# Kernel tuning notes

Hardware: AMD Instinct MI355X
Metric: run time of the kernel (lower is better)

Reference implementation:

```python
import jax, jax.numpy as jnp
import numpy as np

N = 50000      # nodes
E = 640000     # edges
D = 128        # input_dim
H = 128        # hidden_channels
L = 2          # n_layers
NG = 512       # number of graphs
NC = 1         # n_classes
BN_EPS = 1e-5


def _bn(x, gamma, beta):
    # BatchNorm1d over node dim, batch statistics (biased var), eps=1e-5
    mu = jnp.mean(x, axis=0)
    var = jnp.mean((x - mu) ** 2, axis=0)
    return (x - mu) * jax.lax.rsqrt(var + BN_EPS) * gamma + beta


def setup_inputs() -> dict:
    key = jax.random.key(0)
    ks = jax.random.split(key, 16)
    s = 0.05
    x = jax.random.normal(ks[0], (N, D), dtype=jnp.float32)
    edge_index = jax.random.randint(ks[1], (2, E), 0, N, dtype=jnp.int64)
    batch = jnp.sort(jax.random.randint(ks[2], (N,), 0, NG, dtype=jnp.int64))
    return {
        "x": x,
        "edge_index": edge_index,
        "batch": batch,
        "lin_in_w": jax.random.normal(ks[3], (D, H), dtype=jnp.float32) * s,
        "lin_in_b": jnp.zeros((H,), dtype=jnp.float32),
        "mlp_w1": jax.random.normal(ks[4], (L, H, H), dtype=jnp.float32) * s,
        "mlp_b1": jnp.zeros((L, H), dtype=jnp.float32),
        "bn1_g": jnp.ones((L, H), dtype=jnp.float32),
        "bn1_b": jnp.zeros((L, H), dtype=jnp.float32),
        "mlp_w2": jax.random.normal(ks[5], (L, H, H), dtype=jnp.float32) * s,
        "mlp_b2": jnp.zeros((L, H), dtype=jnp.float32),
        "bn_g": jnp.ones((L, H), dtype=jnp.float32),
        "bn_b": jnp.zeros((L, H), dtype=jnp.float32),
        "jk_w": jax.random.normal(ks[6], (L * H, NC), dtype=jnp.float32) * s,
        "jk_b": jnp.zeros((NC,), dtype=jnp.float32),
    }


def reference(x, edge_index, batch, lin_in_w, lin_in_b, mlp_w1, mlp_b1,
              bn1_g, bn1_b, mlp_w2, mlp_b2, bn_g, bn_b, jk_w, jk_b):
    src, dst = edge_index[0], edge_index[1]
    n = x.shape[0]
    h = x @ lin_in_w + lin_in_b  # [N, H]
    outs = []
    for l in range(mlp_w1.shape[0]):
        # GINConv (eps=0): mlp(x + sum_{j in N(i)} x_j)
        agg = jax.ops.segment_sum(h[src], dst, num_segments=n)
        z = h + agg
        z = z @ mlp_w1[l] + mlp_b1[l]
        z = jax.nn.relu(_bn(z, bn1_g[l], bn1_b[l]))
        z = z @ mlp_w2[l] + mlp_b2[l]
        # outer BatchNorm + ReLU; dropout is identity in eval
        h = jax.nn.relu(_bn(z, bn_g[l], bn_b[l]))
        outs.append(h)
    hcat = jnp.concatenate(outs, axis=-1)  # [N, L*H]
    # global mean pool per graph
    counts = jax.ops.segment_sum(jnp.ones((n,), dtype=hcat.dtype), batch, num_segments=NG)
    pooled = jax.ops.segment_sum(hcat, batch, num_segments=NG)
    pooled = pooled / jnp.maximum(counts, 1.0)[:, None]
    return pooled @ jk_w + jk_b  # [NG, n_classes]
```

## Files before the change

### kernel.cpp

```cpp
#include <hip/hip_runtime.h>
#include <cstddef>

#define NN 50000
#define NE 640000
#define NG 512
#define NL 2
#define NSLOT 16
constexpr float BN_EPS = 1e-5f;

typedef __attribute__((ext_vector_type(8))) short bf16x8;
typedef __attribute__((ext_vector_type(16))) float f32x16;

__device__ inline float b2f_lo(unsigned int u) {
  union { unsigned int i; float f; } v; v.i = u << 16; return v.f;
}
__device__ inline float b2f_hi(unsigned int u) {
  union { unsigned int i; float f; } v; v.i = u & 0xffff0000u; return v.f;
}
__device__ inline unsigned short f2b(float f) {
  union { float f; unsigned int i; } v; v.f = f;
  return (unsigned short)((v.i + 0x7fffu + ((v.i >> 16) & 1u)) >> 16);
}
__device__ inline unsigned int pack2(float lo, float hi) {
  return (unsigned int)f2b(lo) | ((unsigned int)f2b(hi) << 16);
}
__device__ inline int swz(int row, int b) { return row * 256 + (b ^ ((row & 15) << 4)); }

__device__ inline void unpack_add(const uint4 v, float* a) {
  a[0] += b2f_lo(v.x); a[1] += b2f_hi(v.x); a[2] += b2f_lo(v.y); a[3] += b2f_hi(v.y);
  a[4] += b2f_lo(v.z); a[5] += b2f_hi(v.z); a[6] += b2f_lo(v.w); a[7] += b2f_hi(v.w);
}

template <int MODE, bool STATS>
__global__ __launch_bounds__(256) void gemm_fused(
    const void* __restrict__ Ain, const float* __restrict__ scale,
    const float* __restrict__ shift, const int* __restrict__ rowptr,
    const int* __restrict__ srcs, const unsigned short* __restrict__ Wt,
    const float* __restrict__ bias, unsigned short* __restrict__ C,
    float* __restrict__ psum, float* __restrict__ psq, int n) {
  __shared__ char Al[16384];
  __shared__ float colsum[128];
  __shared__ float colsq[128];
  const int t = threadIdx.x;
  const int row0 = blockIdx.x * 64;

  if (STATS && t < 128) { colsum[t] = 0.f; colsq[t] = 0.f; }

  if (MODE == 1) {
    const uint4* h4 = (const uint4*)Ain;
    const int ln = t >> 2;
    const int tq = t & 3;
    const int gr = row0 + ln;
    float a[4][8];
    #pragma unroll
    for (int i = 0; i < 4; ++i)
      #pragma unroll
      for (int p = 0; p < 8; ++p) a[i][p] = 0.f;
    if (gr < n) {
      {
        const uint4* p = &h4[(size_t)gr * 16 + tq * 4];
        #pragma unroll
        for (int i = 0; i < 4; ++i) unpack_add(p[i], a[i]);
      }
      const int beg = rowptr[gr], end = rowptr[gr + 1];
      int j = beg;
      for (; j + 1 < end; j += 2) {
        const uint4* p0 = &h4[(size_t)srcs[j] * 16 + tq * 4];
        const uint4* p1 = &h4[(size_t)srcs[j + 1] * 16 + tq * 4];
        const uint4 v00 = p0[0], v01 = p0[1], v02 = p0[2], v03 = p0[3];
        const uint4 v10 = p1[0], v11 = p1[1], v12 = p1[2], v13 = p1[3];
        unpack_add(v00, a[0]); unpack_add(v01, a[1]);
        unpack_add(v02, a[2]); unpack_add(v03, a[3]);
        unpack_add(v10, a[0]); unpack_add(v11, a[1]);
        unpack_add(v12, a[2]); unpack_add(v13, a[3]);
      }
      if (j < end) {
        const uint4* p0 = &h4[(size_t)srcs[j] * 16 + tq * 4];
        #pragma unroll
        for (int i = 0; i < 4; ++i) unpack_add(p0[i], a[i]);
      }
    }
    #pragma unroll
    for (int i = 0; i < 4; ++i) {
      uint4 o;
      o.x = pack2(a[i][0], a[i][1]); o.y = pack2(a[i][2], a[i][3]);
      o.z = pack2(a[i][4], a[i][5]); o.w = pack2(a[i][6], a[i][7]);
      *(uint4*)(Al + swz(ln, (tq * 4 + i) * 16)) = o;
    }
  } else {
    #pragma unroll
    for (int ii = 0; ii < 4; ++ii) {
      const int i = t + ii * 256;
      const int r = i >> 4;
      const int u = (i & 15) << 4;
      const int gr = row0 + r;
      uint4 v = make_uint4(0u, 0u, 0u, 0u);
      if (gr < n) {
        if (MODE == 3) {
          const float* Af = (const float*)Ain;
          const float4 f0 = *(const float4*)(Af + (size_t)gr * 128 + (u >> 1));
          const float4 f1 = *(const float4*)(Af + (size_t)gr * 128 + (u >> 1) + 4);
          v.x = pack2(f0.x, f0.y); v.y = pack2(f0.z, f0.w);
          v.z = pack2(f1.x, f1.y); v.w = pack2(f1.z, f1.w);
        } else {
          v = *(const uint4*)((const char*)Ain + (size_t)gr * 256 + u);
          if (MODE == 2) {
            const int c0 = u >> 1;
            unsigned int pw[4] = {v.x, v.y, v.z, v.w};
            #pragma unroll
            for (int p = 0; p < 4; ++p) {
              float lo = b2f_lo(pw[p]);
              float hi = b2f_hi(pw[p]);
              lo = fmaxf(fmaf(lo, scale[c0 + 2 * p], shift[c0 + 2 * p]), 0.f);
              hi = fmaxf(fmaf(hi, scale[c0 + 2 * p + 1], shift[c0 + 2 * p + 1]), 0.f);
              pw[p] = pack2(lo, hi);
            }
            v = make_uint4(pw[0], pw[1], pw[2], pw[3]);
          }
        }
      }
      *(uint4*)(Al + swz(r, u)) = v;
    }
  }
  __syncthreads();

  const int w = t >> 6;
  const int l = t & 63;
  const int lane31 = l & 31;
  const int khalf = l >> 5;
  const int mrow = (w & 1) * 32;
  const int c0 = (w >> 1) * 64;

  f32x16 acc0, acc1;
  #pragma unroll
  for (int i = 0; i < 16; ++i) { acc0[i] = 0.f; acc1[i] = 0.f; }

  const unsigned short* Bp0 = Wt + (size_t)(c0 + lane31) * 128 + 8 * khalf;
  const unsigned short* Bp1 = Wt + (size_t)(c0 + 32 + lane31) * 128 + 8 * khalf;

  #pragma unroll
  for (int k0 = 0; k0 < 128; k0 += 16) {
    const int kb = (k0 + 8 * khalf) * 2;
    const bf16x8 a  = *(const bf16x8*)(Al + swz(mrow + lane31, kb));
    const bf16x8 b0 = *(const bf16x8*)(Bp0 + k0);
    const bf16x8 b1 = *(const bf16x8*)(Bp1 + k0);
    acc0 = __builtin_amdgcn_mfma_f32_32x32x16_bf16(a, b0, acc0, 0, 0, 0);
    acc1 = __builtin_amdgcn_mfma_f32_32x32x16_bf16(a, b1, acc1, 0, 0, 0);
  }

  const float bias0 = bias[c0 + lane31];
  const float bias1 = bias[c0 + 32 + lane31];
  float s0 = 0.f, q0 = 0.f, s1 = 0.f, q1 = 0.f;
  #pragma unroll
  for (int r = 0; r < 16; ++r) {
    const int row = mrow + (r & 3) + 8 * (r >> 2) + 4 * khalf;
    const int grow = row0 + row;
    if (grow < n) {
      const float v0 = acc0[r] + bias0;
      const float v1 = acc1[r] + bias1;
      C[(size_t)grow * 128 + c0 + lane31] = f2b(v0);
      C[(size_t)grow * 128 + c0 + 32 + lane31] = f2b(v1);
      if (STATS) {
        s0 += v0; q0 = fmaf(v0, v0, q0);
        s1 += v1; q1 = fmaf(v1, v1, q1);
      }
    }
  }
  if (STATS) {
    atomicAdd(&colsum[c0 + lane31], s0);
    atomicAdd(&colsq[c0 + lane31], q0);
    atomicAdd(&colsum[c0 + 32 + lane31], s1);
    atomicAdd(&colsq[c0 + 32 + lane31], q1);
    __syncthreads();
    if (t < 128) {
      const int slot = blockIdx.x & (NSLOT - 1);
      atomicAdd(&psum[slot * 128 + t], colsum[t]);
      atomicAdd(&psq[slot * 128 + t], colsq[t]);
    }
  }
}

__global__ __launch_bounds__(256) void conv_w_k(
    const float* __restrict__ lw, const float* __restrict__ w1,
    const float* __restrict__ w2, unsigned short* __restrict__ Wt) {
  const int i = blockIdx.x * 256 + threadIdx.x;
  if (i >= 5 * 16384) return;
  const int m = i >> 14, r = i & 16383;
  const int ncol = r >> 7, k = r & 127;
  const float* src = (m == 0) ? lw : (m <= 2) ? (w1 + (m - 1) * 16384)
                                              : (w2 + (m - 3) * 16384);
  Wt[i] = f2b(src[k * 128 + ncol]);
}

#define SCAN_B 196
__global__ __launch_bounds__(256) void edge_hist(const int* __restrict__ ei,
                                                 int* __restrict__ cnt) {
  const int e = blockIdx.x * 256 + threadIdx.x;
  if (e >= NE) return;
  atomicAdd(&cnt[ei[NE + e]], 1);
}

__global__ __launch_bounds__(256) void scan1(const int* __restrict__ cnt,
                                             int* __restrict__ rowptr,
                                             int* __restrict__ bsum) {
  __shared__ int s[256];
  const int b = blockIdx.x, t = threadIdx.x;
  const int i = b * 256 + t;
  const int v = (i < NN) ? cnt[i] : 0;
  s[t] = v;
  __syncthreads();
  for (int off = 1; off < 256; off <<= 1) {
    const int x = (t >= off) ? s[t - off] : 0;
    __syncthreads();
    s[t] += x;
    __syncthreads();
  }
  if (i < NN) rowptr[i] = s[t] - v;
  if (t == 255) bsum[b] = s[255];
}

__global__ __launch_bounds__(256) void scan2(const int* __restrict__ bsum,
                                             int* __restrict__ boff,
                                             int* __restrict__ rowptrN) {
  __shared__ int s[256];
  const int t = threadIdx.x;
  const int v = (t < SCAN_B) ? bsum[t] : 0;
  s[t] = v;
  __syncthreads();
  for (int off = 1; off < 256; off <<= 1) {
    const int x = (t >= off) ? s[t - off] : 0;
    __syncthreads();
    s[t] += x;
    __syncthreads();
  }
  if (t < SCAN_B) boff[t] = s[t] - v;
  if (t == 255) *rowptrN = s[255];
}

__global__ __launch_bounds__(256) void scan3(int* __restrict__ rowptr,
                                             const int* __restrict__ boff,
                                             int* __restrict__ cursor) {
  const int i = blockIdx.x * 256 + threadIdx.x;
  if (i < NN) {
    const int v = rowptr[i] + boff[blockIdx.x];
    rowptr[i] = v;
    cursor[i] = v;
  }
}

__global__ __launch_bounds__(256) void build_csr(const int* __restrict__ ei,
                                                 int* __restrict__ cursor,
                                                 int* __restrict__ srcs) {
  const int e = blockIdx.x * 256 + threadIdx.x;
  if (e >= NE) return;
  const int src = ei[e];
  const int dst = ei[NE + e];
  const int pos = atomicAdd(&cursor[dst], 1);
  srcs[pos] = src;
}

__global__ void bn_stats_final(const float* __restrict__ psum,
                               const float* __restrict__ psq,
                               const float* __restrict__ gamma,
                               const float* __restrict__ beta,
                               float* __restrict__ scale,
                               float* __restrict__ shift, int n) {
  const int c = threadIdx.x;
  float s = 0.f, s2 = 0.f;
  #pragma unroll
  for (int b = 0; b < NSLOT; ++b) {
    s += psum[b * 128 + c];
    s2 += psq[b * 128 + c];
  }
  const float inv_n = 1.f / (float)n;
  const float mu = s * inv_n;
  float var = s2 * inv_n - mu * mu;
  var = fmaxf(var, 0.f);
  const float sc = rsqrtf(var + BN_EPS) * gamma[c];
  scale[c] = sc;
  shift[c] = beta[c] - mu * sc;
}

template <bool WRITE_H>
__global__ __launch_bounds__(256) void bn_relu_pool_seg_b(
    const unsigned short* __restrict__ Z, const float* __restrict__ scale,
    const float* __restrict__ shift, const int* __restrict__ gstart,
    unsigned short* __restrict__ h, float* __restrict__ pooled, int layerOff) {
  const int g = blockIdx.x;
  const int r0 = gstart[g], r1 = gstart[g + 1];
  const int t = threadIdx.x;
  const int q = t & 15;
  const int rr = t >> 4;
  const int c0 = q * 8;
  float sc[8], sh[8], acc[8];
  #pragma unroll
  for (int i = 0; i < 8; ++i) { sc[i] = scale[c0 + i]; sh[i] = shift[c0 + i]; acc[i] = 0.f; }
  for (int r = r0 + rr; r < r1; r += 16) {
    const uint4 v = ((const uint4*)Z)[(size_t)r * 16 + q];
    float o[8];
    o[0] = b2f_lo(v.x); o[1] = b2f_hi(v.x); o[2] = b2f_lo(v.y); o[3] = b2f_hi(v.y);
    o[4] = b2f_lo(v.z); o[5] = b2f_hi(v.z); o[6] = b2f_lo(v.w); o[7] = b2f_hi(v.w);
    #pragma unroll
    for (int i = 0; i < 8; ++i) {
      o[i] = fmaxf(fmaf(o[i], sc[i], sh[i]), 0.f);
      acc[i] += o[i];
    }
    if (WRITE_H) {
      uint4 ov;
      ov.x = pack2(o[0], o[1]); ov.y = pack2(o[2], o[3]);
      ov.z = pack2(o[4], o[5]); ov.w = pack2(o[6], o[7]);
      ((uint4*)h)[(size_t)r * 16 + q] = ov;
    }
  }
  __shared__ float red[256 * 8];
  #pragma unroll
  for (int i = 0; i < 8; ++i) red[t * 8 + i] = acc[i];
  __syncthreads();
  for (int off = 8; off >= 1; off >>= 1) {
    if (rr < off) {
      #pragma unroll
      for (int i = 0; i < 8; ++i)
        red[t * 8 + i] += red[(t + off * 16) * 8 + i];
    }
    __syncthreads();
  }
  if (rr == 0) {
    #pragma unroll
    for (int i = 0; i < 8; ++i)
      pooled[(size_t)g * 256 + layerOff + c0 + i] = red[t * 8 + i];
  }
}

__global__ void compute_segments(const int* __restrict__ batch,
                                 int* __restrict__ gstart,
                                 float* __restrict__ counts) {
  const int g = blockIdx.x * blockDim.x + threadIdx.x;
  if (g > NG) return;
  int lo = 0, hi = NN;
  while (lo < hi) { int m = (lo + hi) >> 1; if (batch[m] < g) lo = m + 1; else hi = m; }
  gstart[g] = lo;
  if (g < NG) {
    int lo1 = lo, hi1 = NN;
    while (lo1 < hi1) { int m = (lo1 + hi1) >> 1; if (batch[m] < g + 1) lo1 = m + 1; else hi1 = m; }
    counts[g] = (float)(lo1 - lo);
  }
}

__global__ __launch_bounds__(256) void final_out(
    const float* __restrict__ pooled, const float* __restrict__ counts,
    const float* __restrict__ jkw, const float* __restrict__ jkb,
    float* __restrict__ out) {
  const int wave = threadIdx.x >> 6;
  const int lane = threadIdx.x & 63;
  const int g = blockIdx.x * 4 + wave;
  if (g >= NG) return;
  const float4 p = ((const float4*)(pooled + (size_t)g * 256))[lane];
  const float4 w = ((const float4*)jkw)[lane];
  float s = p.x * w.x + p.y * w.y + p.z * w.z + p.w * w.w;
  for (int off = 32; off; off >>= 1) s += __shfl_down(s, off, 64);
  if (lane == 0) out[g] = s / fmaxf(counts[g], 1.f) + jkb[0];
}

extern "C" void kernel_launch(void* const* d_in, const int* in_sizes, int n_in,
                              void* d_out, int out_size, void* d_ws,
                              size_t ws_size, hipStream_t stream) {
  const float* x     = (const float*)d_in[0];
  const int*   ei    = (const int*)d_in[1];
  const int*   batch = (const int*)d_in[2];
  const float* lin_w = (const float*)d_in[3];
  const float* lin_b = (const float*)d_in[4];
  const float* w1    = (const float*)d_in[5];
  const float* b1    = (const float*)d_in[6];
  const float* g1    = (const float*)d_in[7];
  const float* be1   = (const float*)d_in[8];
  const float* w2    = (const float*)d_in[9];
  const float* b2    = (const float*)d_in[10];
  const float* g2    = (const float*)d_in[11];
  const float* be2   = (const float*)d_in[12];
  const float* jkw   = (const float*)d_in[13];
  const float* jkb   = (const float*)d_in[14];
  float* out = (float*)d_out;

  char* base = (char*)d_ws;
  unsigned short* hb  = (unsigned short*)base;
  unsigned short* agb = hb + (size_t)NN * 128;
  unsigned short* WtA = agb + (size_t)NN * 128;
  float* scale  = (float*)(WtA + 5 * 16384);
  float* shift  = scale + 128;
  float* pooled = shift + 128;
  float* counts = pooled + (size_t)NG * 256;
  int* gstart = (int*)(counts + NG);
  int* rowptr = gstart + NG + 4;
  int* bsum   = rowptr + NN + 4;
  int* boff   = bsum + 200;
  int* srcs   = boff + 200;
  int* cnt    = srcs + NE;
  float* stats = (float*)(cnt + NN);

  hipMemsetAsync(cnt, 0, (size_t)NN * sizeof(int) + 4 * 4096 * sizeof(float),
                 stream);
  conv_w_k<<<(5 * 16384 + 255) / 256, 256, 0, stream>>>(lin_w, w1, w2, WtA);
  compute_segments<<<3, 256, 0, stream>>>(batch, gstart, counts);

  edge_hist<<<(NE + 255) / 256, 256, 0, stream>>>(ei, cnt);
  scan1<<<SCAN_B, 256, 0, stream>>>(cnt, rowptr, bsum);
  scan2<<<1, 256, 0, stream>>>(bsum, boff, rowptr + NN);
  scan3<<<SCAN_B, 256, 0, stream>>>(rowptr, boff, cnt);
  build_csr<<<(NE + 255) / 256, 256, 0, stream>>>(ei, cnt, srcs);

  const int gemm_grid = (NN + 63) / 64;

  gemm_fused<3, false><<<gemm_grid, 256, 0, stream>>>(
      x, nullptr, nullptr, nullptr, nullptr, WtA, lin_b, hb,
      nullptr, nullptr, NN);

  for (int l = 0; l < NL; ++l) {
    float* st1 = stats + (l * 2 + 0) * 4096;
    float* st2 = stats + (l * 2 + 1) * 4096;
    gemm_fused<1, true><<<gemm_grid, 256, 0, stream>>>(
        hb, nullptr, nullptr, rowptr, srcs, WtA + (1 + l) * 16384,
        b1 + l * 128, agb, st1, st1 + 2048, NN);
    bn_stats_final<<<1, 128, 0, stream>>>(st1, st1 + 2048, g1 + l * 128,
                                          be1 + l * 128, scale, shift, NN);
    gemm_fused<2, true><<<gemm_grid, 256, 0, stream>>>(
        agb, scale, shift, nullptr, nullptr, WtA + (3 + l) * 16384,
        b2 + l * 128, agb, st2, st2 + 2048, NN);
    bn_stats_final<<<1, 128, 0, stream>>>(st2, st2 + 2048, g2 + l * 128,
                                          be2 + l * 128, scale, shift, NN);
    if (l + 1 < NL) {
      bn_relu_pool_seg_b<true><<<NG, 256, 0, stream>>>(
          agb, scale, shift, gstart, hb, pooled, l * 128);
    } else {
      bn_relu_pool_seg_b<false><<<NG, 256, 0, stream>>>(
          agb, scale, shift, gstart, hb, pooled, l * 128);
    }
  }

  final_out<<<NG / 4, 256, 0, stream>>>(pooled, counts, jkw, jkb, out);
}
```

Before: 253.0 us.

## Split gather-GEMM into dedicated 32-row kernel with more threads per node

Replaces the MODE 1 gather path of the fused GEMM with a separate kernel that handles 32 rows per block, so each node's neighbour sum is spread over 8 threads of 16 columns each instead of 4 threads of 32 columns. This raises the number of independent gather streams and halves per-thread register accumulators, aiming to hide the latency of the irregular CSR gather. The block doubles its count and does a smaller MFMA tile per wave, so weight reuse per block drops and the stats atomics double.

```diff
diff --git a/kernel.cpp b/kernel.cpp
--- a/kernel.cpp
+++ b/kernel.cpp
@@ -31,11 +31,101 @@
   a[4] += b2f_lo(v.z); a[5] += b2f_hi(v.z); a[6] += b2f_lo(v.w); a[7] += b2f_hi(v.w);
 }
 
+__global__ __launch_bounds__(256) void gemm_gather32(
+    const unsigned short* __restrict__ h, const int* __restrict__ rowptr,
+    const int* __restrict__ srcs, const unsigned short* __restrict__ Wt,
+    const float* __restrict__ bias, unsigned short* __restrict__ C,
+    float* __restrict__ psum, float* __restrict__ psq, int n) {
+  __shared__ uint4 Au[16][32];
+  __shared__ float colsum[128];
+  __shared__ float colsq[128];
+  const int t = threadIdx.x;
+  const int row0 = blockIdx.x * 32;
+
+  if (t < 128) { colsum[t] = 0.f; colsq[t] = 0.f; }
+
+  const int ln = t & 31;
+  const int cg = t >> 5;
+  const int gr = row0 + ln;
+  const uint4* h4 = (const uint4*)h;
+  float a0[8], a1[8];
+  #pragma unroll
+  for (int p = 0; p < 8; ++p) { a0[p] = 0.f; a1[p] = 0.f; }
+  if (gr < n) {
+    {
+      const uint4* p = &h4[(size_t)gr * 16 + cg * 2];
+      unpack_add(p[0], a0); unpack_add(p[1], a1);
+    }
+    const int beg = rowptr[gr], end = rowptr[gr + 1];
+    int j = beg;
+    for (; j + 1 < end; j += 2) {
+      const uint4* p0 = &h4[(size_t)srcs[j] * 16 + cg * 2];
+      const uint4* p1 = &h4[(size_t)srcs[j + 1] * 16 + cg * 2];
+      const uint4 v00 = p0[0], v01 = p0[1];
+      const uint4 v10 = p1[0], v11 = p1[1];
+      unpack_add(v00, a0); unpack_add(v01, a1);
+      unpack_add(v10, a0); unpack_add(v11, a1);
+    }
+    if (j < end) {
+      const uint4* p0 = &h4[(size_t)srcs[j] * 16 + cg * 2];
+      unpack_add(p0[0], a0); unpack_add(p0[1], a1);
+    }
+  }
+  {
+    uint4 o0, o1;
+    o0.x = pack2(a0[0], a0[1]); o0.y = pack2(a0[2], a0[3]);
+    o0.z = pack2(a0[4], a0[5]); o0.w = pack2(a0[6], a0[7]);
+    o1.x = pack2(a1[0], a1[1]); o1.y = pack2(a1[2], a1[3]);
+    o1.z = pack2(a1[4], a1[5]); o1.w = pack2(a1[6], a1[7]);
+    Au[cg * 2][ln] = o0;
+    Au[cg * 2 + 1][ln] = o1;
+  }
+  __syncthreads();
+
+  const int w = t >> 6;
+  const int l = t & 63;
+  const int lane31 = l & 31;
+  const int khalf = l >> 5;
+
+  f32x16 acc;
+  #pragma unroll
+  for (int i = 0; i < 16; ++i) acc[i] = 0.f;
+
+  const unsigned short* Bp = Wt + (size_t)(w * 32 + lane31) * 128 + 8 * khalf;
+  #pragma unroll
+  for (int k0 = 0; k0 < 8; ++k0) {
+    const bf16x8 aF = *(const bf16x8*)&Au[k0 * 2 + khalf][lane31];
+    const bf16x8 bF = *(const bf16x8*)(Bp + k0 * 16);
+    acc = __builtin_amdgcn_mfma_f32_32x32x16_bf16(aF, bF, acc, 0, 0, 0);
+  }
+
+  const int col = w * 32 + lane31;
+  const float bs = bias[col];
+  float s0 = 0.f, q0 = 0.f;
+  #pragma unroll
+  for (int r = 0; r < 16; ++r) {
+    const int row = (r & 3) + 8 * (r >> 2) + 4 * khalf;
+    const int grow = row0 + row;
+    if (grow < n) {
+      const float v = acc[r] + bs;
+      C[(size_t)grow * 128 + col] = f2b(v);
+      s0 += v; q0 = fmaf(v, v, q0);
+    }
+  }
+  atomicAdd(&colsum[col], s0);
+  atomicAdd(&colsq[col], q0);
+  __syncthreads();
+  if (t < 128) {
+    const int slot = blockIdx.x & (NSLOT - 1);
+    atomicAdd(&psum[slot * 128 + t], colsum[t]);
+    atomicAdd(&psq[slot * 128 + t], colsq[t]);
+  }
+}
+
 template <int MODE, bool STATS>
 __global__ __launch_bounds__(256) void gemm_fused(
     const void* __restrict__ Ain, const float* __restrict__ scale,
-    const float* __restrict__ shift, const int* __restrict__ rowptr,
-    const int* __restrict__ srcs, const unsigned short* __restrict__ Wt,
+    const float* __restrict__ shift, const unsigned short* __restrict__ Wt,
     const float* __restrict__ bias, unsigned short* __restrict__ C,
     float* __restrict__ psum, float* __restrict__ psq, int n) {
   __shared__ char Al[16384];
@@ -46,81 +136,36 @@
 
   if (STATS && t < 128) { colsum[t] = 0.f; colsq[t] = 0.f; }
 
-  if (MODE == 1) {
-    const uint4* h4 = (const uint4*)Ain;
-    const int ln = t >> 2;
-    const int tq = t & 3;
-    const int gr = row0 + ln;
-    float a[4][8];
-    #pragma unroll
-    for (int i = 0; i < 4; ++i)
-      #pragma unroll
-      for (int p = 0; p < 8; ++p) a[i][p] = 0.f;
+  #pragma unroll
+  for (int ii = 0; ii < 4; ++ii) {
+    const int i = t + ii * 256;
+    const int r = i >> 4;
+    const int u = (i & 15) << 4;
+    const int gr = row0 + r;
+    uint4 v = make_uint4(0u, 0u, 0u, 0u);
     if (gr < n) {
-      {
-        const uint4* p = &h4[(size_t)gr * 16 + tq * 4];
+      if (MODE == 3) {
+        const float* Af = (const float*)Ain;
+        const float4 f0 = *(const float4*)(Af + (size_t)gr * 128 + (u >> 1));
+        const float4 f1 = *(const float4*)(Af + (size_t)gr * 128 + (u >> 1) + 4);
+        v.x = pack2(f0.x, f0.y); v.y = pack2(f0.z, f0.w);
+        v.z = pack2(f1.x, f1.y); v.w = pack2(f1.z, f1.w);
+      } else {
+        v = *(const uint4*)((const char*)Ain + (size_t)gr * 256 + u);
+        const int c0 = u >> 1;
+        unsigned int pw[4] = {v.x, v.y, v.z, v.w};
         #pragma unroll
-        for (int i = 0; i < 4; ++i) unpack_add(p[i], a[i]);
+        for (int p = 0; p < 4; ++p) {
+          float lo = b2f_lo(pw[p]);
+          float hi = b2f_hi(pw[p]);
+          lo = fmaxf(fmaf(lo, scale[c0 + 2 * p], shift[c0 + 2 * p]), 0.f);
+          hi = fmaxf(fmaf(hi, scale[c0 + 2 * p + 1], shift[c0 + 2 * p + 1]), 0.f);
+          pw[p] = pack2(lo, hi);
+        }
+        v = make_uint4(pw[0], pw[1], pw[2], pw[3]);
       }
-      const int beg = rowptr[gr], end = rowptr[gr + 1];
-      int j = beg;
-      for (; j + 1 < end; j += 2) {
-        const uint4* p0 = &h4[(size_t)srcs[j] * 16 + tq * 4];
-        const uint4* p1 = &h4[(size_t)srcs[j + 1] * 16 + tq * 4];
-        const uint4 v00 = p0[0], v01 = p0[1], v02 = p0[2], v03 = p0[3];
-        const uint4 v10 = p1[0], v11 = p1[1], v12 = p1[2], v13 = p1[3];
-        unpack_add(v00, a[0]); unpack_add(v01, a[1]);
-        unpack_add(v02, a[2]); unpack_add(v03, a[3]);
-        unpack_add(v10, a[0]); unpack_add(v11, a[1]);
-        unpack_add(v12, a[2]); unpack_add(v13, a[3]);
-      }
-      if (j < end) {
-        const uint4* p0 = &h4[(size_t)srcs[j] * 16 + tq * 4];
-        #pragma unroll
-        for (int i = 0; i < 4; ++i) unpack_add(p0[i], a[i]);
-      }
-    }
-    #pragma unroll
-    for (int i = 0; i < 4; ++i) {
-      uint4 o;
-      o.x = pack2(a[i][0], a[i][1]); o.y = pack2(a[i][2], a[i][3]);
-      o.z = pack2(a[i][4], a[i][5]); o.w = pack2(a[i][6], a[i][7]);
-      *(uint4*)(Al + swz(ln, (tq * 4 + i) * 16)) = o;
-    }
-  } else {
-    #pragma unroll
-    for (int ii = 0; ii < 4; ++ii) {
-      const int i = t + ii * 256;
-      const int r = i >> 4;
-      const int u = (i & 15) << 4;
-      const int gr = row0 + r;
-      uint4 v = make_uint4(0u, 0u, 0u, 0u);
-      if (gr < n) {
-        if (MODE == 3) {
-          const float* Af = (const float*)Ain;
-          const float4 f0 = *(const float4*)(Af + (size_t)gr * 128 + (u >> 1));
-          const float4 f1 = *(const float4*)(Af + (size_t)gr * 128 + (u >> 1) + 4);
-          v.x = pack2(f0.x, f0.y); v.y = pack2(f0.z, f0.w);
-          v.z = pack2(f1.x, f1.y); v.w = pack2(f1.z, f1.w);
-        } else {
-          v = *(const uint4*)((const char*)Ain + (size_t)gr * 256 + u);
-          if (MODE == 2) {
-            const int c0 = u >> 1;
-            unsigned int pw[4] = {v.x, v.y, v.z, v.w};
-            #pragma unroll
-            for (int p = 0; p < 4; ++p) {
-              float lo = b2f_lo(pw[p]);
-              float hi = b2f_hi(pw[p]);
-              lo = fmaxf(fmaf(lo, scale[c0 + 2 * p], shift[c0 + 2 * p]), 0.f);
-              hi = fmaxf(fmaf(hi, scale[c0 + 2 * p + 1], shift[c0 + 2 * p + 1]), 0.f);
-              pw[p] = pack2(lo, hi);
-            }
-            v = make_uint4(pw[0], pw[1], pw[2], pw[3]);
-          }
-        }
-      }
-      *(uint4*)(Al + swz(r, u)) = v;
-    }
+    }
+    *(uint4*)(Al + swz(r, u)) = v;
   }
   __syncthreads();
 
@@ -409,22 +454,22 @@
   build_csr<<<(NE + 255) / 256, 256, 0, stream>>>(ei, cnt, srcs);
 
   const int gemm_grid = (NN + 63) / 64;
+  const int gath_grid = (NN + 31) / 32;
 
   gemm_fused<3, false><<<gemm_grid, 256, 0, stream>>>(
-      x, nullptr, nullptr, nullptr, nullptr, WtA, lin_b, hb,
-      nullptr, nullptr, NN);
+      x, nullptr, nullptr, WtA, lin_b, hb, nullptr, nullptr, NN);
 
   for (int l = 0; l < NL; ++l) {
     float* st1 = stats + (l * 2 + 0) * 4096;
     float* st2 = stats + (l * 2 + 1) * 4096;
-    gemm_fused<1, true><<<gemm_grid, 256, 0, stream>>>(
-        hb, nullptr, nullptr, rowptr, srcs, WtA + (1 + l) * 16384,
-        b1 + l * 128, agb, st1, st1 + 2048, NN);
+    gemm_gather32<<<gath_grid, 256, 0, stream>>>(
+        hb, rowptr, srcs, WtA + (1 + l) * 16384, b1 + l * 128, agb,
+        st1, st1 + 2048, NN);
     bn_stats_final<<<1, 128, 0, stream>>>(st1, st1 + 2048, g1 + l * 128,
                                           be1 + l * 128, scale, shift, NN);
     gemm_fused<2, true><<<gemm_grid, 256, 0, stream>>>(
-        agb, scale, shift, nullptr, nullptr, WtA + (3 + l) * 16384,
-        b2 + l * 128, agb, st2, st2 + 2048, NN);
+        agb, scale, shift, WtA + (3 + l) * 16384, b2 + l * 128, agb,
+        st2, st2 + 2048, NN);
     bn_stats_final<<<1, 128, 0, stream>>>(st2, st2 + 2048, g2 + l * 128,
                                           be2 + l * 128, scale, shift, NN);
     if (l + 1 < NL) {
```

New measurement: 258.7 us. 1.02x slower.
